# Kernel tuning notes

Measured on AMD Instinct MI355X. Metric: run time of the kernel, lower is better.

Reference implementation:

```python
import jax, jax.numpy as jnp
import numpy as np
import math
from jax import lax

S = 2048   # layer_size (number of neurons)
T = 384    # timesteps per forward call
ALPHA = 0.15
DT = 0.1
THRESH = -50.0
V_RESET = -70.0
VL = -70.0
GL = 0.025
CM = 0.5
TAU = CM / GL                                   # 20.0
COEF = DT ** ALPHA * math.gamma(2.0 - ALPHA) / CM  # dt^alpha * Gamma(2-alpha) / Cm


def setup_inputs() -> dict:
    key = jax.random.key(0)
    I_old = jax.random.normal(key, (S, T), dtype=jnp.float32)
    # class-level fractional (Grunwald-Letnikov style) weight vector, x=5000
    x = 5000
    nv = np.arange(x - 1)
    w = ((x - nv + 1) ** (1.0 - ALPHA) - (x - nv) ** (1.0 - ALPHA)).astype(np.float32)
    return {"I_old": I_old, "weights": jnp.asarray(w)}


def _forward(I_old, weights):
    S_, T_ = I_old.shape
    dtype = I_old.dtype
    # wr[a] = weights[-a]: the memory weight applied to a delta that is `a` steps old.
    # Original: np.inner(weights[-N+1:], delta_trace) pairs oldest delta with weights[-(N-1)]
    # and the newest delta with weights[-1].
    wr = jnp.concatenate([jnp.zeros((1,), dtype), weights[::-1][:T_].astype(dtype)])  # [T+1]
    jidx = jnp.arange(T_)  # buffer slot j holds the delta appended at global step j

    def step(carry, xs):
        V, buf = carry          # V: [S], buf: [S, T] delta history (slot j = delta of step j)
        n, I_n = xs             # n: scalar step index, I_n: [S]
        # fractional memory term: sum_{j=1}^{n-1} wr[n-j] * delta_j
        ages = n - jidx                                        # [T]
        coeff = jnp.where((ages >= 1) & (jidx >= 1),
                          wr[jnp.clip(ages, 0, T_)], jnp.zeros((), dtype))  # [T]
        memory = buf @ coeff                                   # [S]
        # three update rules depending on the global step counter
        V1 = V + (DT / TAU) * (-V + I_n / GL)                  # N == 1 branch
        V2 = COEF * (-GL * (V - VL) + I_n) + V - memory        # N >= 2 branch
        V_pre = jnp.where(n == 0, jnp.full_like(V, -70.0),
                          jnp.where(n == 1, V1, V2))
        spike = (V - THRESH > 0).astype(dtype)                 # spike uses PREVIOUS V
        reset = lax.stop_gradient(spike * (THRESH - V_RESET))  # detached reset
        V_new = V_pre - reset
        buf = buf.at[:, n].set(V_new - V)                      # append delta (n=0 slot masked out)
        return (V_new, buf), (spike, V_new)

    V0 = jnp.zeros((S_,), dtype)          # V_trace initialized to 0 per neuron
    buf0 = jnp.zeros((S_, T_), dtype)
    (_, _), (spk, trc) = lax.scan(step, (V0, buf0), (jnp.arange(T_), I_old.T))
    return spk.T, trc.T                    # each [S, T]


def reference(I_old, weights):
    return _forward(I_old, weights)
```

## Files before the change

### kernel.cpp

```cpp
#include <hip/hip_runtime.h>
#include <cmath>

#define T_STEPS 384
#define CH 64
#define NCH 6
#define WS 392

__device__ __forceinline__ float readlane_f(float v, int l) {
    return __int_as_float(__builtin_amdgcn_readlane(__float_as_int(v), l));
}

__global__ __launch_bounds__(128, 4)
void flif_kernel(const float* __restrict__ I_old, const float* __restrict__ W,
                 float* __restrict__ out, float cm1, float c2, float c3, int Stot)
{
    const int tid  = threadIdx.x;
    const int wid  = tid >> 6;
    const int lane = tid & 63;
    const int s    = blockIdx.x;

    __shared__ __align__(16) float wtr[4 * WS];
    __shared__ __align__(16) float lrep[4 * 128];
    __shared__ __align__(16) float dbuf[T_STEPS];
    __shared__ float accs[2][CH];

    for (int k = tid; k < 4 * WS; k += 128) {
        const int r = k / WS, kk = k - r * WS;
        const int i = kk + r;
        wtr[k] = (i <= 382) ? W[4998 - i] : 0.0f;
    }
    for (int k = tid; k < 512; k += 128) {
        const int r = k >> 7, kk = k & 127;
        const int x = kk + r;
        lrep[k] = (x >= 64 && x <= 126) ? W[5062 - x] : 0.0f;
    }
    ((float*)accs)[tid] = 0.0f;
    __syncthreads();

    const int rl = lane & 3;
    const float* wlp = wtr + rl * WS + (lane - rl);

    if (wid == 1) {
        for (int c = 0; c < NCH; ++c) {
            if (c >= 1 && c <= 4) {
                const int CB = (c + 1) * CH;
                float acc = 0.0f;
                #pragma unroll 2
                for (int m0 = CB - 4; m0 >= 64; m0 -= 4) {
                    const float4 d4 = *reinterpret_cast<const float4*>(dbuf + (CB - m0 - 4));
                    const float4 w4 = *reinterpret_cast<const float4*>(wlp + m0);
                    acc = fmaf(d4.x, w4.w, acc);
                    acc = fmaf(d4.y, w4.z, acc);
                    acc = fmaf(d4.z, w4.y, acc);
                    acc = fmaf(d4.w, w4.x, acc);
                }
                accs[(c + 1) & 1][lane] = acc;
            }
            __syncthreads();
        }
        return;
    }

    const float* Irow = I_old + (size_t)s * T_STEPS;
    float Inext = Irow[lane];

    float wloc[64];
    {
        const int r = lane & 3;
        const float* lp = lrep + r * 128 - r;
        #pragma unroll
        for (int i0 = 0; i0 < 64; i0 += 4) {
            const float4 f = *reinterpret_cast<const float4*>(lp + (lane + 60 - i0));
            wloc[i0 + 0] = f.w; wloc[i0 + 1] = f.z;
            wloc[i0 + 2] = f.y; wloc[i0 + 3] = f.x;
        }
    }

    const float wr1n = -W[4998];

    float V = 0.0f, d = 0.0f, b = 0.0f, P = 0.0f;
    float tcs[NCH], spks[NCH];

    for (int c = 0; c < NCH; ++c) {
        const int cb = c * CH;
        const float Ic = Inext;
        if (c + 1 < NCH) Inext = Irow[cb + CH + lane];

        float acc = accs[c & 1][lane];
        if (c >= 1) {
            #pragma unroll 2
            for (int m0 = 60; m0 >= 0; m0 -= 4) {
                const float4 d4 = *reinterpret_cast<const float4*>(dbuf + (cb - m0 - 4));
                const float4 w4 = *reinterpret_cast<const float4*>(wlp + m0);
                acc = fmaf(d4.x, w4.w, acc);
                acc = fmaf(d4.y, w4.z, acc);
                acc = fmaf(d4.z, w4.y, acc);
                acc = fmaf(d4.w, w4.x, acc);
            }
        }

        float u = fmaf(c3, Ic, c2) - acc;
        const float Vs = V;
        float tc = 0.0f;

        auto body = [&](int i) {
            const float t = fmaf(wr1n, d, P);
            d = t + b;
            P = readlane_f(u, (i + 1) & 63);
            V = V + d;
            const float rv = (V > -50.0f) ? -20.0f : 0.0f;
            b = fmaf(cm1, V, rv);
            u = fmaf(-wloc[i], d, u);
            tc = (lane == i) ? V : tc;
        };

        if (c == 0) {
            V = -90.0f;
            if (lane == 0) tc = V;
            const float I1 = readlane_f(Ic, 1);
            const float V1 = fmaf(0.005f, (I1 / 0.025f) - V, V);
            const float d1 = V1 - V;
            P = readlane_f(u, 2);
            u = fmaf(-wloc[1], d1, u);
            if (lane == 1) tc = V1;
            V = V1;
            d = d1;
            const float rv = (V > -50.0f) ? -20.0f : 0.0f;
            b = fmaf(cm1, V, rv);
            #pragma unroll
            for (int i = 2; i < CH; ++i) body(i);
        } else {
            d = 0.0f;
            P = readlane_f(u, 0);
            #pragma unroll
            for (int i = 0; i < CH; ++i) body(i);
        }

        float prev = __shfl_up(tc, 1);
        if (lane == 0) prev = Vs;
        spks[c] = (prev > -50.0f) ? 1.0f : 0.0f;
        float dd = tc - prev;
        if (c == 0 && lane == 0) dd = 0.0f;
        dbuf[cb + lane] = dd;
        tcs[c] = tc;
        __syncthreads();
    }

    float* out_spk = out + (size_t)s * T_STEPS;
    float* out_trc = out + (size_t)Stot * T_STEPS + (size_t)s * T_STEPS;
    #pragma unroll
    for (int c = 0; c < NCH; ++c) {
        out_spk[c * CH + lane] = spks[c];
        out_trc[c * CH + lane] = tcs[c];
    }
}

extern "C" void kernel_launch(void* const* d_in, const int* in_sizes, int n_in,
                              void* d_out, int out_size, void* d_ws, size_t ws_size,
                              hipStream_t stream) {
    const float* I = (const float*)d_in[0];
    const float* W = (const float*)d_in[1];
    float* out = (float*)d_out;
    const int S = in_sizes[0] / T_STEPS;

    const double COEF = std::pow(0.1, 0.15) * std::tgamma(1.85) / 0.5;
    const float c3  = (float)COEF;
    const float cm1 = (float)(-COEF * 0.025);
    const float c2  = (float)(COEF * 0.025 * -70.0);

    flif_kernel<<<S, 128, 0, stream>>>(I, W, out, cm1, c2, c3, S);
}
```

Before: 85.09 us.

## Replace per-lane weight register array with DPP wave shift; batch helper-wave accumulation

The 64-entry per-lane weight array (wloc) and its LDS staging table are replaced by a single register that is shifted one lane per step with a DPP row/wave shift-right, cutting register pressure and setup LDS traffic. The helper wave now reads each freshly produced delta chunk once and accumulates its contribution into all future chunk accumulators (A2..A5) at the same time, instead of rereading the whole growing history for every chunk. The main wave's first-chunk accumulator read is skipped and its history loop is fully unrolled. In exchange, each sequential step gains an extra cross-lane DPP move, and the helper wave holds more live accumulators.

Measured after the change: 80.74 us. 1.05x faster.

```diff
diff --git a/kernel.cpp b/kernel.cpp
--- a/kernel.cpp
+++ b/kernel.cpp
@@ -10,6 +10,10 @@
     return __int_as_float(__builtin_amdgcn_readlane(__float_as_int(v), l));
 }
 
+__device__ __forceinline__ float wave_shr1_f(float v) {
+    return __int_as_float(__builtin_amdgcn_mov_dpp(__float_as_int(v), 0x138, 0xf, 0xf, true));
+}
+
 __global__ __launch_bounds__(128, 4)
 void flif_kernel(const float* __restrict__ I_old, const float* __restrict__ W,
                  float* __restrict__ out, float cm1, float c2, float c3, int Stot)
@@ -20,7 +24,6 @@
     const int s    = blockIdx.x;
 
     __shared__ __align__(16) float wtr[4 * WS];
-    __shared__ __align__(16) float lrep[4 * 128];
     __shared__ __align__(16) float dbuf[T_STEPS];
     __shared__ float accs[2][CH];
 
@@ -29,11 +32,6 @@
         const int i = kk + r;
         wtr[k] = (i <= 382) ? W[4998 - i] : 0.0f;
     }
-    for (int k = tid; k < 512; k += 128) {
-        const int r = k >> 7, kk = k & 127;
-        const int x = kk + r;
-        lrep[k] = (x >= 64 && x <= 126) ? W[5062 - x] : 0.0f;
-    }
     ((float*)accs)[tid] = 0.0f;
     __syncthreads();
 
@@ -41,20 +39,28 @@
     const float* wlp = wtr + rl * WS + (lane - rl);
 
     if (wid == 1) {
+        float A2 = 0.0f, A3 = 0.0f, A4 = 0.0f, A5 = 0.0f;
+        #pragma unroll
         for (int c = 0; c < NCH; ++c) {
             if (c >= 1 && c <= 4) {
-                const int CB = (c + 1) * CH;
-                float acc = 0.0f;
-                #pragma unroll 2
-                for (int m0 = CB - 4; m0 >= 64; m0 -= 4) {
-                    const float4 d4 = *reinterpret_cast<const float4*>(dbuf + (CB - m0 - 4));
-                    const float4 w4 = *reinterpret_cast<const float4*>(wlp + m0);
-                    acc = fmaf(d4.x, w4.w, acc);
-                    acc = fmaf(d4.y, w4.z, acc);
-                    acc = fmaf(d4.z, w4.y, acc);
-                    acc = fmaf(d4.w, w4.x, acc);
+                const int src = c - 1;
+                const float* dp = dbuf + src * CH;
+                #pragma unroll
+                for (int k = 0; k <= 60; k += 4) {
+                    const float4 d4 = *reinterpret_cast<const float4*>(dp + k);
+                    #pragma unroll
+                    for (int t = c + 1; t <= 5; ++t) {
+                        const int g = t - src;
+                        const float4 w4 = *reinterpret_cast<const float4*>(wlp + (g * 64 - k - 4));
+                        float& At = (t == 2) ? A2 : (t == 3) ? A3 : (t == 4) ? A4 : A5;
+                        At = fmaf(d4.x, w4.w, At);
+                        At = fmaf(d4.y, w4.z, At);
+                        At = fmaf(d4.z, w4.y, At);
+                        At = fmaf(d4.w, w4.x, At);
+                    }
                 }
-                accs[(c + 1) & 1][lane] = acc;
+                const float hand = (c == 1) ? A2 : (c == 2) ? A3 : (c == 3) ? A4 : A5;
+                accs[(c + 1) & 1][lane] = hand;
             }
             __syncthreads();
         }
@@ -63,19 +69,7 @@
 
     const float* Irow = I_old + (size_t)s * T_STEPS;
     float Inext = Irow[lane];
-
-    float wloc[64];
-    {
-        const int r = lane & 3;
-        const float* lp = lrep + r * 128 - r;
-        #pragma unroll
-        for (int i0 = 0; i0 < 64; i0 += 4) {
-            const float4 f = *reinterpret_cast<const float4*>(lp + (lane + 60 - i0));
-            wloc[i0 + 0] = f.w; wloc[i0 + 1] = f.z;
-            wloc[i0 + 2] = f.y; wloc[i0 + 3] = f.x;
-        }
-    }
-
+    const float w0   = (lane >= 1) ? W[4999 - lane] : 0.0f;
     const float wr1n = -W[4998];
 
     float V = 0.0f, d = 0.0f, b = 0.0f, P = 0.0f;
@@ -86,11 +80,12 @@
         const float Ic = Inext;
         if (c + 1 < NCH) Inext = Irow[cb + CH + lane];
 
-        float acc = accs[c & 1][lane];
+        float acc = (c == 0) ? 0.0f : accs[c & 1][lane];
         if (c >= 1) {
-            #pragma unroll 2
+            const float* dp = dbuf + (c - 1) * CH;
+            #pragma unroll
             for (int m0 = 60; m0 >= 0; m0 -= 4) {
-                const float4 d4 = *reinterpret_cast<const float4*>(dbuf + (cb - m0 - 4));
+                const float4 d4 = *reinterpret_cast<const float4*>(dp + (60 - m0));
                 const float4 w4 = *reinterpret_cast<const float4*>(wlp + m0);
                 acc = fmaf(d4.x, w4.w, acc);
                 acc = fmaf(d4.y, w4.z, acc);
@@ -102,6 +97,7 @@
         float u = fmaf(c3, Ic, c2) - acc;
         const float Vs = V;
         float tc = 0.0f;
+        float w = w0;
 
         auto body = [&](int i) {
             const float t = fmaf(wr1n, d, P);
@@ -110,18 +106,21 @@
             V = V + d;
             const float rv = (V > -50.0f) ? -20.0f : 0.0f;
             b = fmaf(cm1, V, rv);
-            u = fmaf(-wloc[i], d, u);
+            u = fmaf(-w, d, u);
+            w = wave_shr1_f(w);
             tc = (lane == i) ? V : tc;
         };
 
         if (c == 0) {
             V = -90.0f;
             if (lane == 0) tc = V;
+            w = wave_shr1_f(w);
             const float I1 = readlane_f(Ic, 1);
             const float V1 = fmaf(0.005f, (I1 / 0.025f) - V, V);
             const float d1 = V1 - V;
             P = readlane_f(u, 2);
-            u = fmaf(-wloc[1], d1, u);
+            u = fmaf(-w, d1, u);
+            w = wave_shr1_f(w);
             if (lane == 1) tc = V1;
             V = V1;
             d = d1;
```
